# Performance work log

Hardware: AMD Instinct MI355X
Metric: run time of the kernel (lower is better)

## Reference

```python
import jax, jax.numpy as jnp
import numpy as np

B, S, D = 4, 2048, 1024
DFF = 512
E = 16
TOP_K = 2
N_SHARED = 2
FUSED_DFF = DFF * N_SHARED


def setup_inputs() -> dict:
    key = jax.random.key(0)
    ks = jax.random.split(key, 16)
    sc_d = 1.0 / np.sqrt(D)
    sc_f = 1.0 / np.sqrt(DFF)
    sc_sf = 1.0 / np.sqrt(FUSED_DFF)
    inp = {
        "x": jax.random.normal(ks[0], (B, S, D), dtype=jnp.float32),
        "gate_w": jax.random.uniform(ks[1], (E, D), dtype=jnp.float32, minval=-sc_d, maxval=sc_d),
        "expert_bias": jnp.zeros((E,), dtype=jnp.float32),
        # routed experts (SwiGLU): w1,w3: [E, DFF, D], w2: [E, D, DFF]
        "w1": jax.random.uniform(ks[2], (E, DFF, D), dtype=jnp.float32, minval=-sc_d, maxval=sc_d),
        "b1": jax.random.uniform(ks[3], (E, DFF), dtype=jnp.float32, minval=-sc_d, maxval=sc_d),
        "w3": jax.random.uniform(ks[4], (E, DFF, D), dtype=jnp.float32, minval=-sc_d, maxval=sc_d),
        "b3": jax.random.uniform(ks[5], (E, DFF), dtype=jnp.float32, minval=-sc_d, maxval=sc_d),
        "w2": jax.random.uniform(ks[6], (E, D, DFF), dtype=jnp.float32, minval=-sc_f, maxval=sc_f),
        "b2": jax.random.uniform(ks[7], (E, D), dtype=jnp.float32, minval=-sc_f, maxval=sc_f),
        # fused shared experts: d_model -> 2*d_ff -> d_model
        "sw1": jax.random.uniform(ks[8], (FUSED_DFF, D), dtype=jnp.float32, minval=-sc_d, maxval=sc_d),
        "sb1": jax.random.uniform(ks[9], (FUSED_DFF,), dtype=jnp.float32, minval=-sc_d, maxval=sc_d),
        "sw3": jax.random.uniform(ks[10], (FUSED_DFF, D), dtype=jnp.float32, minval=-sc_d, maxval=sc_d),
        "sb3": jax.random.uniform(ks[11], (FUSED_DFF,), dtype=jnp.float32, minval=-sc_d, maxval=sc_d),
        "sw2": jax.random.uniform(ks[12], (D, FUSED_DFF), dtype=jnp.float32, minval=-sc_sf, maxval=sc_sf),
        "sb2": jax.random.uniform(ks[13], (D,), dtype=jnp.float32, minval=-sc_sf, maxval=sc_sf),
    }
    return inp


def reference(x, gate_w, expert_bias, w1, b1, w2, b2, w3, b3,
              sw1, sb1, sw2, sb2, sw3, sb3):
    Bv, Sv, Dv = x.shape
    xf = x.reshape(-1, Dv)                                  # [T, D]
    # --- Gate (sigmoid scores, top-k over bias-adjusted logits) ---
    logits = xf @ gate_w.T                                  # [T, E]
    scores = jax.nn.sigmoid(logits)
    biased = logits + expert_bias.astype(logits.dtype)[None, :]
    _, topk_idx = jax.lax.top_k(biased, TOP_K)              # [T, K]
    topk_w = jnp.take_along_axis(scores, topk_idx, axis=-1) # [T, K]
    topk_w = topk_w / (topk_w.sum(-1, keepdims=True) + 1e-10)
    # dense per-token per-expert combine weight (zero for unselected) [T, E]
    gatew = (jax.nn.one_hot(topk_idx, E, dtype=xf.dtype) * topk_w[..., None]).sum(1)
    # --- Routed experts: equivalent to sort/dispatch/grouped-GEMM/combine ---
    y = jnp.zeros_like(xf)
    for e in range(E):
        h = jax.nn.silu(xf @ w1[e].T + b1[e]) * (xf @ w3[e].T + b3[e])  # [T, DFF]
        y = y + gatew[:, e:e + 1] * (h @ w2[e].T + b2[e])
    # --- Fused shared experts ---
    hs = jax.nn.silu(xf @ sw1.T + sb1) * (xf @ sw3.T + sb3)             # [T, 2*DFF]
    y = y + hs @ sw2.T + sb2
    return y.reshape(Bv, Sv, Dv)
```

## Files before the change

### kernel.cpp

```cpp
#include <hip/hip_runtime.h>
#include <cstdint>
#include <cstddef>

#define DEV static __device__ __forceinline__

constexpr int TT   = 8192;
constexpr int DD   = 1024;
constexpr int DFF  = 512;
constexpr int NE   = 16;
constexpr int FDFF = 1024;
constexpr int NSLOT = TT * 2;
constexpr int NSLOT_PAD = NSLOT + NE * 128;
constexpr int MAXT = NSLOT / 128 + NE;
constexpr int HB   = 64;

constexpr size_t XB_OFF   = 0;
constexpr size_t HS_OFF   = XB_OFF  + (size_t)TT * DD * 2;
constexpr size_t HR_OFF   = HS_OFF  + (size_t)TT * FDFF * 2;
constexpr size_t W1B_OFF  = HR_OFF  + (size_t)NSLOT_PAD * DFF * 2;
constexpr size_t W3B_OFF  = W1B_OFF + (size_t)NE * DFF * DD * 2;
constexpr size_t W2B_OFF  = W3B_OFF + (size_t)NE * DFF * DD * 2;
constexpr size_t SW1B_OFF = W2B_OFF + (size_t)NE * DD * DFF * 2;
constexpr size_t SW3B_OFF = SW1B_OFF + (size_t)FDFF * DD * 2;
constexpr size_t SW2B_OFF = SW3B_OFF + (size_t)FDFF * DD * 2;
constexpr size_t TKI_OFF  = SW2B_OFF + (size_t)DD * FDFF * 2;
constexpr size_t TKW_OFF  = TKI_OFF + (size_t)NSLOT * 4;
constexpr size_t STOK_OFF = TKW_OFF + (size_t)NSLOT * 4;
constexpr size_t SWT_OFF  = STOK_OFF + (size_t)NSLOT_PAD * 4;
constexpr size_t LRK_OFF  = SWT_OFF + (size_t)NSLOT_PAD * 4;
constexpr size_t BCN_OFF  = LRK_OFF + (size_t)NSLOT * 4;
constexpr size_t BB_OFF   = BCN_OFF + (size_t)HB * NE * 4;
constexpr size_t OFS_OFF  = BB_OFF + (size_t)HB * NE * 4;
constexpr size_t TEX_OFF  = OFS_OFF + 128;
constexpr size_t TM0_OFF  = TEX_OFF + (size_t)MAXT * 4;

typedef __bf16 bf16x8 __attribute__((ext_vector_type(8)));
typedef float  floatx4 __attribute__((ext_vector_type(4)));
typedef unsigned short u16t;

DEV unsigned f2bf2(float lo, float hi) {
    unsigned a = __builtin_bit_cast(unsigned, lo);
    unsigned b = __builtin_bit_cast(unsigned, hi);
    a += 0x7FFFu + ((a >> 16) & 1u);
    b += 0x7FFFu + ((b >> 16) & 1u);
    return (a >> 16) | (b & 0xFFFF0000u);
}
DEV u16t f2bf1(float f) {
    unsigned u = __builtin_bit_cast(unsigned, f);
    u += 0x7FFFu + ((u >> 16) & 1u);
    return (u16t)(u >> 16);
}
DEV uint4 pack8(float4 a, float4 b) {
    uint4 r;
    r.x = f2bf2(a.x, a.y); r.y = f2bf2(a.z, a.w);
    r.z = f2bf2(b.x, b.y); r.w = f2bf2(b.z, b.w);
    return r;
}
DEV floatx4 mfma16(bf16x8 a, bf16x8 b, floatx4 c) {
    return __builtin_amdgcn_mfma_f32_16x16x32_bf16(a, b, c, 0, 0, 0);
}
DEV void glds16(const u16t* g, u16t* l) {
    __builtin_amdgcn_global_load_lds(
        (const __attribute__((address_space(1))) unsigned int*)g,
        (__attribute__((address_space(3))) unsigned int*)l, 16, 0, 0);
}
DEV float dot4(float4 a, float4 b) { return a.x*b.x + a.y*b.y + a.z*b.z + a.w*b.w; }

__global__ __launch_bounds__(256) void k_cvtw(
        const float* __restrict__ w1, const float* __restrict__ w3, const float* __restrict__ w2,
        const float* __restrict__ sw1, const float* __restrict__ sw3, const float* __restrict__ sw2,
        u16t* __restrict__ w1b, u16t* __restrict__ w3b, u16t* __restrict__ w2b,
        u16t* __restrict__ sw1b, u16t* __restrict__ sw3b, u16t* __restrict__ sw2b) {
    int b = blockIdx.x;
    const float* src; u16t* dst; size_t base;
    if      (b < 4096)  { src = w1;  dst = w1b;  base = (size_t)b * 2048; }
    else if (b < 8192)  { src = w3;  dst = w3b;  base = (size_t)(b - 4096) * 2048; }
    else if (b < 12288) { src = w2;  dst = w2b;  base = (size_t)(b - 8192) * 2048; }
    else if (b < 12800) { src = sw1; dst = sw1b; base = (size_t)(b - 12288) * 2048; }
    else if (b < 13312) { src = sw3; dst = sw3b; base = (size_t)(b - 12800) * 2048; }
    else                { src = sw2; dst = sw2b; base = (size_t)(b - 13312) * 2048; }
    size_t i = base + (size_t)threadIdx.x * 8;
    float4 a = *(const float4*)(src + i);
    float4 c = *(const float4*)(src + i + 4);
    *(uint4*)(dst + i) = pack8(a, c);
}

__global__ __launch_bounds__(256) void k_cvtx(const float* __restrict__ x, u16t* __restrict__ xb) {
    size_t i = ((size_t)blockIdx.x * 256 + threadIdx.x) * 8;
    float4 a = *(const float4*)(x + i);
    float4 b = *(const float4*)(x + i + 4);
    *(uint4*)(xb + i) = pack8(a, b);
}

__global__ __launch_bounds__(256) void k_gate(const float* __restrict__ x,
                                              const float* __restrict__ gw,
                                              const float* __restrict__ eb,
                                              int* __restrict__ tki, float* __restrict__ tkw) {
    const int tid = threadIdx.x;
    const int wave = tid >> 6, lane = tid & 63;
    const int tok0 = blockIdx.x * 16 + wave * 4;
    float acc[4][16];
#pragma unroll
    for (int t = 0; t < 4; t++)
#pragma unroll
        for (int e = 0; e < 16; e++) acc[t][e] = 0.f;
#pragma unroll
    for (int i = 0; i < 4; i++) {
        const int d = i * 256 + lane * 4;
        float4 xv[4];
#pragma unroll
        for (int t = 0; t < 4; t++) xv[t] = *(const float4*)(x + (size_t)(tok0 + t) * DD + d);
#pragma unroll
        for (int e = 0; e < 16; e++) {
            float4 wv = *(const float4*)(gw + (size_t)e * DD + d);
#pragma unroll
            for (int t = 0; t < 4; t++) acc[t][e] += dot4(xv[t], wv);
        }
    }
#pragma unroll
    for (int t = 0; t < 4; t++)
#pragma unroll
        for (int e = 0; e < 16; e++) {
            float v = acc[t][e];
            v += __shfl_xor(v, 1);  v += __shfl_xor(v, 2);  v += __shfl_xor(v, 4);
            v += __shfl_xor(v, 8);  v += __shfl_xor(v, 16); v += __shfl_xor(v, 32);
            acc[t][e] = v;
        }
    if (lane == 0) {
        float ebs[16];
#pragma unroll
        for (int e = 0; e < 16; e++) ebs[e] = eb[e];
#pragma unroll
        for (int t = 0; t < 4; t++) {
            float b0 = -1e30f, b1v = -1e30f, l0 = 0.f, l1 = 0.f;
            int i0 = 0, i1 = 0;
#pragma unroll
            for (int e = 0; e < 16; e++) {
                float lv = acc[t][e];
                float bl = lv + ebs[e];
                if (bl > b0)       { b1v = b0; i1 = i0; l1 = l0; b0 = bl; i0 = e; l0 = lv; }
                else if (bl > b1v) { b1v = bl; i1 = e; l1 = lv; }
            }
            float s0 = 1.f / (1.f + expf(-l0));
            float s1 = 1.f / (1.f + expf(-l1));
            float dn = s0 + s1 + 1e-10f;
            int tok = tok0 + t;
            tki[tok * 2] = i0; tki[tok * 2 + 1] = i1;
            tkw[tok * 2] = s0 / dn; tkw[tok * 2 + 1] = s1 / dn;
        }
    }
}

__global__ __launch_bounds__(256) void k_hist(const int* __restrict__ tki,
                                              int* __restrict__ lrank, int* __restrict__ bcnt) {
    __shared__ int h[NE];
    const int tid = threadIdx.x;
    if (tid < NE) h[tid] = 0;
    __syncthreads();
    int idx = blockIdx.x * 256 + tid;
    int e = tki[idx];
    lrank[idx] = atomicAdd(&h[e], 1);
    __syncthreads();
    if (tid < NE) bcnt[blockIdx.x * NE + tid] = h[tid];
}

__global__ void k_scan(const int* __restrict__ bcnt, int* __restrict__ offs,
                       int* __restrict__ bb, int* __restrict__ texp, int* __restrict__ tm0) {
    __shared__ int cntS[NE], offS[NE];
    const int tid = threadIdx.x;
    if (tid < NE) {
        int s = 0;
#pragma unroll
        for (int b = 0; b < HB; b++) s += bcnt[b * NE + tid];
        cntS[tid] = s;
    }
    __syncthreads();
    if (tid == 0) {
        int off = 0, t = 0;
        for (int e = 0; e < NE; e++) {
            offS[e] = off; offs[e] = off;
            int nt = (cntS[e] + 127) >> 7;
            for (int i = 0; i < nt; i++) { texp[t] = e; tm0[t] = off + i * 128; t++; }
            off += nt * 128;
        }
        offs[NE] = off;
        for (; t < MAXT; t++) texp[t] = -1;
    }
    __syncthreads();
    if (tid < NE) {
        int run = offS[tid];
        for (int b = 0; b < HB; b++) { bb[b * NE + tid] = run; run += bcnt[b * NE + tid]; }
    }
}

__global__ __launch_bounds__(256) void k_scatter(const int* __restrict__ tki,
                                                 const float* __restrict__ tkw,
                                                 const int* __restrict__ bb,
                                                 const int* __restrict__ lrank,
                                                 int* __restrict__ stok, float* __restrict__ swt) {
    int idx = blockIdx.x * 256 + threadIdx.x;
    int e = tki[idx];
    int slot = bb[blockIdx.x * NE + e] + lrank[idx];
    stok[slot] = idx >> 1;
    swt[slot] = tkw[idx];
}

__global__ __launch_bounds__(256) void k_sgemm1(const u16t* __restrict__ xb,
        const u16t* __restrict__ w1b, const float* __restrict__ sb1,
        const u16t* __restrict__ w3b, const float* __restrict__ sb3,
        u16t* __restrict__ Hs) {
    __shared__ u16t As[128 * 32], B1s[64 * 32], B3s[64 * 32];
    const int m0 = blockIdx.x * 128, n0 = blockIdx.y * 64;
    const int tid = threadIdx.x, lane = tid & 63, wid = tid >> 6;
    const int wm = (wid & 1) * 64, wn = (wid >> 1) * 32;
    const int q = lane >> 4, r = lane & 15;
    const int srow = tid >> 2, scg = (tid & 3) * 8;
    floatx4 acc1[4][2], acc3[4][2];
#pragma unroll
    for (int i = 0; i < 4; i++)
#pragma unroll
        for (int j = 0; j < 2; j++) { acc1[i][j] = (floatx4)0.f; acc3[i][j] = (floatx4)0.f; }
    const u16t* a0  = xb  + (size_t)(m0 + srow) * DD + scg;
    const u16t* a1  = xb  + (size_t)(m0 + 64 + srow) * DD + scg;
    const u16t* b1g = w1b + (size_t)(n0 + srow) * DD + scg;
    const u16t* b3g = w3b + (size_t)(n0 + srow) * DD + scg;
    u16t* lA0 = As + tid * 8;
    u16t* lA1 = As + 2048 + tid * 8;
    u16t* lB1 = B1s + tid * 8;
    u16t* lB3 = B3s + tid * 8;
    for (int k0 = 0; k0 < DD; k0 += 32) {
        glds16(a0 + k0, lA0); glds16(a1 + k0, lA1);
        glds16(b1g + k0, lB1); glds16(b3g + k0, lB3);
        __syncthreads();
        bf16x8 af[4], f1[2], f3[2];
#pragma unroll
        for (int i = 0; i < 4; i++) af[i] = *(const bf16x8*)&As[(wm + i * 16 + r) * 32 + q * 8];
#pragma unroll
        for (int j = 0; j < 2; j++) {
            f1[j] = *(const bf16x8*)&B1s[(wn + j * 16 + r) * 32 + q * 8];
            f3[j] = *(const bf16x8*)&B3s[(wn + j * 16 + r) * 32 + q * 8];
        }
#pragma unroll
        for (int i = 0; i < 4; i++)
#pragma unroll
            for (int j = 0; j < 2; j++) {
                acc1[i][j] = mfma16(af[i], f1[j], acc1[i][j]);
                acc3[i][j] = mfma16(af[i], f3[j], acc3[i][j]);
            }
        __syncthreads();
    }
    float s1v[2], s3v[2];
#pragma unroll
    for (int j = 0; j < 2; j++) {
        int col = n0 + wn + j * 16 + r;
        s1v[j] = sb1[col]; s3v[j] = sb3[col];
    }
#pragma unroll
    for (int i = 0; i < 4; i++)
#pragma unroll
        for (int j = 0; j < 2; j++)
#pragma unroll
            for (int g = 0; g < 4; g++) {
                int row = m0 + wm + i * 16 + q * 4 + g;
                int col = n0 + wn + j * 16 + r;
                float z1 = acc1[i][j][g] + s1v[j];
                float z3 = acc3[i][j][g] + s3v[j];
                float h = (z1 / (1.f + __expf(-z1))) * z3;
                Hs[(size_t)row * FDFF + col] = f2bf1(h);
            }
}

__global__ __launch_bounds__(256) void k_sgemm2(const u16t* __restrict__ Hs,
        const u16t* __restrict__ sw2b, const float* __restrict__ sb2,
        float* __restrict__ out) {
    __shared__ u16t As[128 * 32], Bs[128 * 32];
    const int m0 = blockIdx.x * 128, n0 = blockIdx.y * 128;
    const int tid = threadIdx.x, lane = tid & 63, wid = tid >> 6;
    const int wm = (wid & 1) * 64, wn = (wid >> 1) * 64;
    const int q = lane >> 4, r = lane & 15;
    const int srow = tid >> 2, scg = (tid & 3) * 8;
    floatx4 acc[4][4];
#pragma unroll
    for (int i = 0; i < 4; i++)
#pragma unroll
        for (int j = 0; j < 4; j++) acc[i][j] = (floatx4)0.f;
    const u16t* a0 = Hs + (size_t)(m0 + srow) * FDFF + scg;
    const u16t* a1 = Hs + (size_t)(m0 + 64 + srow) * FDFF + scg;
    const u16t* b0 = sw2b + (size_t)(n0 + srow) * FDFF + scg;
    const u16t* b1 = sw2b + (size_t)(n0 + 64 + srow) * FDFF + scg;
    u16t* lA0 = As + tid * 8;       u16t* lA1 = As + 2048 + tid * 8;
    u16t* lB0 = Bs + tid * 8;       u16t* lB1 = Bs + 2048 + tid * 8;
    for (int k0 = 0; k0 < FDFF; k0 += 32) {
        glds16(a0 + k0, lA0); glds16(a1 + k0, lA1);
        glds16(b0 + k0, lB0); glds16(b1 + k0, lB1);
        __syncthreads();
        bf16x8 af[4], bf[4];
#pragma unroll
        for (int i = 0; i < 4; i++) af[i] = *(const bf16x8*)&As[(wm + i * 16 + r) * 32 + q * 8];
#pragma unroll
        for (int j = 0; j < 4; j++) bf[j] = *(const bf16x8*)&Bs[(wn + j * 16 + r) * 32 + q * 8];
#pragma unroll
        for (int i = 0; i < 4; i++)
#pragma unroll
            for (int j = 0; j < 4; j++) acc[i][j] = mfma16(af[i], bf[j], acc[i][j]);
        __syncthreads();
    }
    float bv[4];
#pragma unroll
    for (int j = 0; j < 4; j++) bv[j] = sb2[n0 + wn + j * 16 + r];
#pragma unroll
    for (int i = 0; i < 4; i++)
#pragma unroll
        for (int j = 0; j < 4; j++)
#pragma unroll
            for (int g = 0; g < 4; g++) {
                int row = m0 + wm + i * 16 + q * 4 + g;
                int col = n0 + wn + j * 16 + r;
                out[(size_t)row * DD + col] = acc[i][j][g] + bv[j];
            }
}

__global__ __launch_bounds__(256) void k_rgemm1(const u16t* __restrict__ xb,
        const u16t* __restrict__ w1b, const float* __restrict__ b1,
        const u16t* __restrict__ w3b, const float* __restrict__ b3,
        const int* __restrict__ stok,
        const int* __restrict__ texp, const int* __restrict__ tm0,
        u16t* __restrict__ Hr) {
    const int te = texp[blockIdx.x];
    if (te < 0) return;
    const int m0 = tm0[blockIdx.x], n0 = blockIdx.y * 64;
    __shared__ u16t As[128 * 32], B1s[64 * 32], B3s[64 * 32];
    __shared__ int toksS[128];
    const int tid = threadIdx.x, lane = tid & 63, wid = tid >> 6;
    const int wm = (wid & 1) * 64, wn = (wid >> 1) * 32;
    const int q = lane >> 4, r = lane & 15;
    const int srow = tid >> 2, scg = (tid & 3) * 8;
    if (tid < 128) { int t = stok[m0 + tid]; toksS[tid] = t < 0 ? 0 : t; }
    __syncthreads();
    floatx4 acc1[4][2], acc3[4][2];
#pragma unroll
    for (int i = 0; i < 4; i++)
#pragma unroll
        for (int j = 0; j < 2; j++) { acc1[i][j] = (floatx4)0.f; acc3[i][j] = (floatx4)0.f; }
    const u16t* a0  = xb + (size_t)toksS[srow] * DD + scg;
    const u16t* a1  = xb + (size_t)toksS[64 + srow] * DD + scg;
    const u16t* b1g = w1b + (size_t)te * DFF * DD + (size_t)(n0 + srow) * DD + scg;
    const u16t* b3g = w3b + (size_t)te * DFF * DD + (size_t)(n0 + srow) * DD + scg;
    const float* b1e = b1 + (size_t)te * DFF;
    const float* b3e = b3 + (size_t)te * DFF;
    u16t* lA0 = As + tid * 8;
    u16t* lA1 = As + 2048 + tid * 8;
    u16t* lB1 = B1s + tid * 8;
    u16t* lB3 = B3s + tid * 8;
    for (int k0 = 0; k0 < DD; k0 += 32) {
        glds16(a0 + k0, lA0); glds16(a1 + k0, lA1);
        glds16(b1g + k0, lB1); glds16(b3g + k0, lB3);
        __syncthreads();
        bf16x8 af[4], f1[2], f3[2];
#pragma unroll
        for (int i = 0; i < 4; i++) af[i] = *(const bf16x8*)&As[(wm + i * 16 + r) * 32 + q * 8];
#pragma unroll
        for (int j = 0; j < 2; j++) {
            f1[j] = *(const bf16x8*)&B1s[(wn + j * 16 + r) * 32 + q * 8];
            f3[j] = *(const bf16x8*)&B3s[(wn + j * 16 + r) * 32 + q * 8];
        }
#pragma unroll
        for (int i = 0; i < 4; i++)
#pragma unroll
            for (int j = 0; j < 2; j++) {
                acc1[i][j] = mfma16(af[i], f1[j], acc1[i][j]);
                acc3[i][j] = mfma16(af[i], f3[j], acc3[i][j]);
            }
        __syncthreads();
    }
    float s1v[2], s3v[2];
#pragma unroll
    for (int j = 0; j < 2; j++) {
        int col = n0 + wn + j * 16 + r;
        s1v[j] = b1e[col]; s3v[j] = b3e[col];
    }
#pragma unroll
    for (int i = 0; i < 4; i++)
#pragma unroll
        for (int j = 0; j < 2; j++)
#pragma unroll
            for (int g = 0; g < 4; g++) {
                int slot = m0 + wm + i * 16 + q * 4 + g;
                int col = n0 + wn + j * 16 + r;
                float z1 = acc1[i][j][g] + s1v[j];
                float z3 = acc3[i][j][g] + s3v[j];
                float h = (z1 / (1.f + __expf(-z1))) * z3;
                Hr[(size_t)slot * DFF + col] = f2bf1(h);
            }
}

__global__ __launch_bounds__(256) void k_rgemm2(const u16t* __restrict__ Hr,
        const u16t* __restrict__ w2b, const float* __restrict__ b2,
        const int* __restrict__ stok, const float* __restrict__ swt,
        const int* __restrict__ texp, const int* __restrict__ tm0,
        float* __restrict__ out) {
    const int te = texp[blockIdx.x];
    if (te < 0) return;
    const int m0 = tm0[blockIdx.x], n0 = blockIdx.y * 128;
    __shared__ u16t As[128 * 32], Bs[128 * 32];
    __shared__ int toksR[128];
    __shared__ float swtL[128];
    const int tid = threadIdx.x, lane = tid & 63, wid = tid >> 6;
    const int wm = (wid & 1) * 64, wn = (wid >> 1) * 64;
    const int q = lane >> 4, r = lane & 15;
    const int srow = tid >> 2, scg = (tid & 3) * 8;
    if (tid < 128) { toksR[tid] = stok[m0 + tid]; swtL[tid] = swt[m0 + tid]; }
    floatx4 acc[4][4];
#pragma unroll
    for (int i = 0; i < 4; i++)
#pragma unroll
        for (int j = 0; j < 4; j++) acc[i][j] = (floatx4)0.f;
    const u16t* a0 = Hr + (size_t)(m0 + srow) * DFF + scg;
    const u16t* a1 = Hr + (size_t)(m0 + 64 + srow) * DFF + scg;
    const u16t* b0 = w2b + (size_t)te * DD * DFF + (size_t)(n0 + srow) * DFF + scg;
    const u16t* b1 = w2b + (size_t)te * DD * DFF + (size_t)(n0 + 64 + srow) * DFF + scg;
    const float* b2e = b2 + (size_t)te * DD;
    u16t* lA0 = As + tid * 8;       u16t* lA1 = As + 2048 + tid * 8;
    u16t* lB0 = Bs + tid * 8;       u16t* lB1 = Bs + 2048 + tid * 8;
    for (int k0 = 0; k0 < DFF; k0 += 32) {
        glds16(a0 + k0, lA0); glds16(a1 + k0, lA1);
        glds16(b0 + k0, lB0); glds16(b1 + k0, lB1);
        __syncthreads();
        bf16x8 af[4], bf[4];
#pragma unroll
        for (int i = 0; i < 4; i++) af[i] = *(const bf16x8*)&As[(wm + i * 16 + r) * 32 + q * 8];
#pragma unroll
        for (int j = 0; j < 4; j++) bf[j] = *(const bf16x8*)&Bs[(wn + j * 16 + r) * 32 + q * 8];
#pragma unroll
        for (int i = 0; i < 4; i++)
#pragma unroll
            for (int j = 0; j < 4; j++) acc[i][j] = mfma16(af[i], bf[j], acc[i][j]);
        __syncthreads();
    }
    float bv[4];
#pragma unroll
    for (int j = 0; j < 4; j++) bv[j] = b2e[n0 + wn + j * 16 + r];
#pragma unroll
    for (int i = 0; i < 4; i++)
#pragma unroll
        for (int g = 0; g < 4; g++) {
            int rowl = wm + i * 16 + q * 4 + g;
            int tk = toksR[rowl];
            if (tk >= 0) {
                float gwv = swtL[rowl];
#pragma unroll
                for (int j = 0; j < 4; j++) {
                    int col = n0 + wn + j * 16 + r;
                    atomicAdd(out + (size_t)tk * DD + col, gwv * (acc[i][j][g] + bv[j]));
                }
            }
        }
}

extern "C" void kernel_launch(void* const* d_in, const int* in_sizes, int n_in,
                              void* d_out, int out_size, void* d_ws, size_t ws_size,
                              hipStream_t stream) {
    const float* x   = (const float*)d_in[0];
    const float* gw  = (const float*)d_in[1];
    const float* eb  = (const float*)d_in[2];
    const float* w1  = (const float*)d_in[3];
    const float* b1  = (const float*)d_in[4];
    const float* w3  = (const float*)d_in[5];
    const float* b3  = (const float*)d_in[6];
    const float* w2  = (const float*)d_in[7];
    const float* b2  = (const float*)d_in[8];
    const float* sw1 = (const float*)d_in[9];
    const float* sb1 = (const float*)d_in[10];
    const float* sw3 = (const float*)d_in[11];
    const float* sb3 = (const float*)d_in[12];
    const float* sw2 = (const float*)d_in[13];
    const float* sb2 = (const float*)d_in[14];
    float* out = (float*)d_out;
    char* ws = (char*)d_ws;

    u16t*  xb   = (u16t*)(ws + XB_OFF);
    u16t*  Hs   = (u16t*)(ws + HS_OFF);
    u16t*  Hr   = (u16t*)(ws + HR_OFF);
    u16t*  w1b  = (u16t*)(ws + W1B_OFF);
    u16t*  w3b  = (u16t*)(ws + W3B_OFF);
    u16t*  w2b  = (u16t*)(ws + W2B_OFF);
    u16t*  sw1b = (u16t*)(ws + SW1B_OFF);
    u16t*  sw3b = (u16t*)(ws + SW3B_OFF);
    u16t*  sw2b = (u16t*)(ws + SW2B_OFF);
    int*   tki  = (int*)(ws + TKI_OFF);
    float* tkw  = (float*)(ws + TKW_OFF);
    int*   stok = (int*)(ws + STOK_OFF);
    float* swt  = (float*)(ws + SWT_OFF);
    int*   lrank = (int*)(ws + LRK_OFF);
    int*   bcnt = (int*)(ws + BCN_OFF);
    int*   bb   = (int*)(ws + BB_OFF);
    int*   offs = (int*)(ws + OFS_OFF);
    int*   texp = (int*)(ws + TEX_OFF);
    int*   tm0  = (int*)(ws + TM0_OFF);

    hipMemsetAsync(stok, 0xFF, (size_t)NSLOT_PAD * 4, stream);

    k_cvtw<<<13824, 256, 0, stream>>>(w1, w3, w2, sw1, sw3, sw2, w1b, w3b, w2b, sw1b, sw3b, sw2b);
    k_cvtx<<<4096, 256, 0, stream>>>(x, xb);
    k_gate<<<512, 256, 0, stream>>>(x, gw, eb, tki, tkw);
    k_hist<<<HB, 256, 0, stream>>>(tki, lrank, bcnt);
    k_scan<<<1, 64, 0, stream>>>(bcnt, offs, bb, texp, tm0);
    k_scatter<<<HB, 256, 0, stream>>>(tki, tkw, bb, lrank, stok, swt);

    k_sgemm1<<<dim3(TT / 128, FDFF / 64), 256, 0, stream>>>(xb, sw1b, sb1, sw3b, sb3, Hs);
    k_sgemm2<<<dim3(TT / 128, DD / 128), 256, 0, stream>>>(Hs, sw2b, sb2, out);
    k_rgemm1<<<dim3(MAXT, DFF / 64), 256, 0, stream>>>(xb, w1b, b1, w3b, b3, stok, texp, tm0, Hr);
    k_rgemm2<<<dim3(MAXT, DD / 128), 256, 0, stream>>>(Hr, w2b, b2, stok, swt, texp, tm0, out);
}
```

Measured before the change: 462.0 us.

## Swizzle LDS tile layout for conflict-free fragment reads; replace atomic combine with gather kernel

The global-to-LDS load mapping is changed so each 16-row group is stored contiguously by k-chunk, letting the MFMA fragment reads hit consecutive addresses instead of 64-byte-strided rows. This targets LDS bank conflicts in all four GEMM kernels. In addition, the routed down-projection now writes bf16 per-slot results to a new buffer. A separate combine kernel then gathers each token's two slots, applies bias and gate weights, and adds them to the output without float atomics. The trade is an extra intermediate buffer write/read, one more launch, and bf16 rounding of the routed output before combining.

```diff
diff --git a/kernel.cpp b/kernel.cpp
--- a/kernel.cpp
+++ b/kernel.cpp
@@ -17,7 +17,8 @@
 constexpr size_t XB_OFF   = 0;
 constexpr size_t HS_OFF   = XB_OFF  + (size_t)TT * DD * 2;
 constexpr size_t HR_OFF   = HS_OFF  + (size_t)TT * FDFF * 2;
-constexpr size_t W1B_OFF  = HR_OFF  + (size_t)NSLOT_PAD * DFF * 2;
+constexpr size_t YR_OFF   = HR_OFF  + (size_t)NSLOT_PAD * DFF * 2;
+constexpr size_t W1B_OFF  = YR_OFF  + (size_t)NSLOT_PAD * DD * 2;
 constexpr size_t W3B_OFF  = W1B_OFF + (size_t)NE * DFF * DD * 2;
 constexpr size_t W2B_OFF  = W3B_OFF + (size_t)NE * DFF * DD * 2;
 constexpr size_t SW1B_OFF = W2B_OFF + (size_t)NE * DD * DFF * 2;
@@ -26,8 +27,8 @@
 constexpr size_t TKI_OFF  = SW2B_OFF + (size_t)DD * FDFF * 2;
 constexpr size_t TKW_OFF  = TKI_OFF + (size_t)NSLOT * 4;
 constexpr size_t STOK_OFF = TKW_OFF + (size_t)NSLOT * 4;
-constexpr size_t SWT_OFF  = STOK_OFF + (size_t)NSLOT_PAD * 4;
-constexpr size_t LRK_OFF  = SWT_OFF + (size_t)NSLOT_PAD * 4;
+constexpr size_t PSL_OFF  = STOK_OFF + (size_t)NSLOT_PAD * 4;
+constexpr size_t LRK_OFF  = PSL_OFF + (size_t)NSLOT * 4;
 constexpr size_t BCN_OFF  = LRK_OFF + (size_t)NSLOT * 4;
 constexpr size_t BB_OFF   = BCN_OFF + (size_t)HB * NE * 4;
 constexpr size_t OFS_OFF  = BB_OFF + (size_t)HB * NE * 4;
@@ -50,6 +51,7 @@
     u += 0x7FFFu + ((u >> 16) & 1u);
     return (u16t)(u >> 16);
 }
+DEV float bf2f(u16t v) { unsigned u = (unsigned)v << 16; return __builtin_bit_cast(float, u); }
 DEV uint4 pack8(float4 a, float4 b) {
     uint4 r;
     r.x = f2bf2(a.x, a.y); r.y = f2bf2(a.z, a.w);
@@ -194,16 +196,18 @@
 }
 
 __global__ __launch_bounds__(256) void k_scatter(const int* __restrict__ tki,
-                                                 const float* __restrict__ tkw,
                                                  const int* __restrict__ bb,
                                                  const int* __restrict__ lrank,
-                                                 int* __restrict__ stok, float* __restrict__ swt) {
+                                                 int* __restrict__ stok, int* __restrict__ pslot) {
     int idx = blockIdx.x * 256 + threadIdx.x;
     int e = tki[idx];
     int slot = bb[blockIdx.x * NE + e] + lrank[idx];
     stok[slot] = idx >> 1;
-    swt[slot] = tkw[idx];
-}
+    pslot[idx] = slot;
+}
+
+#define LROW(tid) ((((tid) >> 6) << 4) | ((tid) & 15))
+#define LCG(tid)  ((((tid) >> 4) & 3) * 8)
 
 __global__ __launch_bounds__(256) void k_sgemm1(const u16t* __restrict__ xb,
         const u16t* __restrict__ w1b, const float* __restrict__ sb1,
@@ -214,31 +218,32 @@
     const int tid = threadIdx.x, lane = tid & 63, wid = tid >> 6;
     const int wm = (wid & 1) * 64, wn = (wid >> 1) * 32;
     const int q = lane >> 4, r = lane & 15;
-    const int srow = tid >> 2, scg = (tid & 3) * 8;
+    const int lrow = LROW(tid), lcg = LCG(tid);
     floatx4 acc1[4][2], acc3[4][2];
 #pragma unroll
     for (int i = 0; i < 4; i++)
 #pragma unroll
         for (int j = 0; j < 2; j++) { acc1[i][j] = (floatx4)0.f; acc3[i][j] = (floatx4)0.f; }
-    const u16t* a0  = xb  + (size_t)(m0 + srow) * DD + scg;
-    const u16t* a1  = xb  + (size_t)(m0 + 64 + srow) * DD + scg;
-    const u16t* b1g = w1b + (size_t)(n0 + srow) * DD + scg;
-    const u16t* b3g = w3b + (size_t)(n0 + srow) * DD + scg;
+    const u16t* a0  = xb  + (size_t)(m0 + lrow) * DD + lcg;
+    const u16t* a1  = xb  + (size_t)(m0 + 64 + lrow) * DD + lcg;
+    const u16t* b1g = w1b + (size_t)(n0 + lrow) * DD + lcg;
+    const u16t* b3g = w3b + (size_t)(n0 + lrow) * DD + lcg;
     u16t* lA0 = As + tid * 8;
     u16t* lA1 = As + 2048 + tid * 8;
     u16t* lB1 = B1s + tid * 8;
     u16t* lB3 = B3s + tid * 8;
+    const int ag = (wm >> 4), bg = (wn >> 4);
     for (int k0 = 0; k0 < DD; k0 += 32) {
         glds16(a0 + k0, lA0); glds16(a1 + k0, lA1);
         glds16(b1g + k0, lB1); glds16(b3g + k0, lB3);
         __syncthreads();
         bf16x8 af[4], f1[2], f3[2];
 #pragma unroll
-        for (int i = 0; i < 4; i++) af[i] = *(const bf16x8*)&As[(wm + i * 16 + r) * 32 + q * 8];
+        for (int i = 0; i < 4; i++) af[i] = *(const bf16x8*)&As[(ag + i) * 512 + q * 128 + r * 8];
 #pragma unroll
         for (int j = 0; j < 2; j++) {
-            f1[j] = *(const bf16x8*)&B1s[(wn + j * 16 + r) * 32 + q * 8];
-            f3[j] = *(const bf16x8*)&B3s[(wn + j * 16 + r) * 32 + q * 8];
+            f1[j] = *(const bf16x8*)&B1s[(bg + j) * 512 + q * 128 + r * 8];
+            f3[j] = *(const bf16x8*)&B3s[(bg + j) * 512 + q * 128 + r * 8];
         }
 #pragma unroll
         for (int i = 0; i < 4; i++)
@@ -278,27 +283,28 @@
     const int tid = threadIdx.x, lane = tid & 63, wid = tid >> 6;
     const int wm = (wid & 1) * 64, wn = (wid >> 1) * 64;
     const int q = lane >> 4, r = lane & 15;
-    const int srow = tid >> 2, scg = (tid & 3) * 8;
+    const int lrow = LROW(tid), lcg = LCG(tid);
     floatx4 acc[4][4];
 #pragma unroll
     for (int i = 0; i < 4; i++)
 #pragma unroll
         for (int j = 0; j < 4; j++) acc[i][j] = (floatx4)0.f;
-    const u16t* a0 = Hs + (size_t)(m0 + srow) * FDFF + scg;
-    const u16t* a1 = Hs + (size_t)(m0 + 64 + srow) * FDFF + scg;
-    const u16t* b0 = sw2b + (size_t)(n0 + srow) * FDFF + scg;
-    const u16t* b1 = sw2b + (size_t)(n0 + 64 + srow) * FDFF + scg;
+    const u16t* a0 = Hs + (size_t)(m0 + lrow) * FDFF + lcg;
+    const u16t* a1 = Hs + (size_t)(m0 + 64 + lrow) * FDFF + lcg;
+    const u16t* b0 = sw2b + (size_t)(n0 + lrow) * FDFF + lcg;
+    const u16t* b1 = sw2b + (size_t)(n0 + 64 + lrow) * FDFF + lcg;
     u16t* lA0 = As + tid * 8;       u16t* lA1 = As + 2048 + tid * 8;
     u16t* lB0 = Bs + tid * 8;       u16t* lB1 = Bs + 2048 + tid * 8;
+    const int ag = (wm >> 4), bg = (wn >> 4);
     for (int k0 = 0; k0 < FDFF; k0 += 32) {
         glds16(a0 + k0, lA0); glds16(a1 + k0, lA1);
         glds16(b0 + k0, lB0); glds16(b1 + k0, lB1);
         __syncthreads();
         bf16x8 af[4], bf[4];
 #pragma unroll
-        for (int i = 0; i < 4; i++) af[i] = *(const bf16x8*)&As[(wm + i * 16 + r) * 32 + q * 8];
-#pragma unroll
-        for (int j = 0; j < 4; j++) bf[j] = *(const bf16x8*)&Bs[(wn + j * 16 + r) * 32 + q * 8];
+        for (int i = 0; i < 4; i++) af[i] = *(const bf16x8*)&As[(ag + i) * 512 + q * 128 + r * 8];
+#pragma unroll
+        for (int j = 0; j < 4; j++) bf[j] = *(const bf16x8*)&Bs[(bg + j) * 512 + q * 128 + r * 8];
 #pragma unroll
         for (int i = 0; i < 4; i++)
 #pragma unroll
@@ -334,7 +340,7 @@
     const int tid = threadIdx.x, lane = tid & 63, wid = tid >> 6;
     const int wm = (wid & 1) * 64, wn = (wid >> 1) * 32;
     const int q = lane >> 4, r = lane & 15;
-    const int srow = tid >> 2, scg = (tid & 3) * 8;
+    const int lrow = LROW(tid), lcg = LCG(tid);
     if (tid < 128) { int t = stok[m0 + tid]; toksS[tid] = t < 0 ? 0 : t; }
     __syncthreads();
     floatx4 acc1[4][2], acc3[4][2];
@@ -342,27 +348,28 @@
     for (int i = 0; i < 4; i++)
 #pragma unroll
         for (int j = 0; j < 2; j++) { acc1[i][j] = (floatx4)0.f; acc3[i][j] = (floatx4)0.f; }
-    const u16t* a0  = xb + (size_t)toksS[srow] * DD + scg;
-    const u16t* a1  = xb + (size_t)toksS[64 + srow] * DD + scg;
-    const u16t* b1g = w1b + (size_t)te * DFF * DD + (size_t)(n0 + srow) * DD + scg;
-    const u16t* b3g = w3b + (size_t)te * DFF * DD + (size_t)(n0 + srow) * DD + scg;
+    const u16t* a0  = xb + (size_t)toksS[lrow] * DD + lcg;
+    const u16t* a1  = xb + (size_t)toksS[64 + lrow] * DD + lcg;
+    const u16t* b1g = w1b + (size_t)te * DFF * DD + (size_t)(n0 + lrow) * DD + lcg;
+    const u16t* b3g = w3b + (size_t)te * DFF * DD + (size_t)(n0 + lrow) * DD + lcg;
     const float* b1e = b1 + (size_t)te * DFF;
     const float* b3e = b3 + (size_t)te * DFF;
     u16t* lA0 = As + tid * 8;
     u16t* lA1 = As + 2048 + tid * 8;
     u16t* lB1 = B1s + tid * 8;
     u16t* lB3 = B3s + tid * 8;
+    const int ag = (wm >> 4), bg = (wn >> 4);
     for (int k0 = 0; k0 < DD; k0 += 32) {
         glds16(a0 + k0, lA0); glds16(a1 + k0, lA1);
         glds16(b1g + k0, lB1); glds16(b3g + k0, lB3);
         __syncthreads();
         bf16x8 af[4], f1[2], f3[2];
 #pragma unroll
-        for (int i = 0; i < 4; i++) af[i] = *(const bf16x8*)&As[(wm + i * 16 + r) * 32 + q * 8];
+        for (int i = 0; i < 4; i++) af[i] = *(const bf16x8*)&As[(ag + i) * 512 + q * 128 + r * 8];
 #pragma unroll
         for (int j = 0; j < 2; j++) {
-            f1[j] = *(const bf16x8*)&B1s[(wn + j * 16 + r) * 32 + q * 8];
-            f3[j] = *(const bf16x8*)&B3s[(wn + j * 16 + r) * 32 + q * 8];
+            f1[j] = *(const bf16x8*)&B1s[(bg + j) * 512 + q * 128 + r * 8];
+            f3[j] = *(const bf16x8*)&B3s[(bg + j) * 512 + q * 128 + r * 8];
         }
 #pragma unroll
         for (int i = 0; i < 4; i++)
@@ -395,66 +402,75 @@
 }
 
 __global__ __launch_bounds__(256) void k_rgemm2(const u16t* __restrict__ Hr,
-        const u16t* __restrict__ w2b, const float* __restrict__ b2,
-        const int* __restrict__ stok, const float* __restrict__ swt,
+        const u16t* __restrict__ w2b,
         const int* __restrict__ texp, const int* __restrict__ tm0,
-        float* __restrict__ out) {
+        u16t* __restrict__ Yr) {
     const int te = texp[blockIdx.x];
     if (te < 0) return;
     const int m0 = tm0[blockIdx.x], n0 = blockIdx.y * 128;
     __shared__ u16t As[128 * 32], Bs[128 * 32];
-    __shared__ int toksR[128];
-    __shared__ float swtL[128];
     const int tid = threadIdx.x, lane = tid & 63, wid = tid >> 6;
     const int wm = (wid & 1) * 64, wn = (wid >> 1) * 64;
     const int q = lane >> 4, r = lane & 15;
-    const int srow = tid >> 2, scg = (tid & 3) * 8;
-    if (tid < 128) { toksR[tid] = stok[m0 + tid]; swtL[tid] = swt[m0 + tid]; }
+    const int lrow = LROW(tid), lcg = LCG(tid);
     floatx4 acc[4][4];
 #pragma unroll
     for (int i = 0; i < 4; i++)
 #pragma unroll
         for (int j = 0; j < 4; j++) acc[i][j] = (floatx4)0.f;
-    const u16t* a0 = Hr + (size_t)(m0 + srow) * DFF + scg;
-    const u16t* a1 = Hr + (size_t)(m0 + 64 + srow) * DFF + scg;
-    const u16t* b0 = w2b + (size_t)te * DD * DFF + (size_t)(n0 + srow) * DFF + scg;
-    const u16t* b1 = w2b + (size_t)te * DD * DFF + (size_t)(n0 + 64 + srow) * DFF + scg;
-    const float* b2e = b2 + (size_t)te * DD;
+    const u16t* a0 = Hr + (size_t)(m0 + lrow) * DFF + lcg;
+    const u16t* a1 = Hr + (size_t)(m0 + 64 + lrow) * DFF + lcg;
+    const u16t* b0 = w2b + (size_t)te * DD * DFF + (size_t)(n0 + lrow) * DFF + lcg;
+    const u16t* b1 = w2b + (size_t)te * DD * DFF + (size_t)(n0 + 64 + lrow) * DFF + lcg;
     u16t* lA0 = As + tid * 8;       u16t* lA1 = As + 2048 + tid * 8;
     u16t* lB0 = Bs + tid * 8;       u16t* lB1 = Bs + 2048 + tid * 8;
+    const int ag = (wm >> 4), bg = (wn >> 4);
     for (int k0 = 0; k0 < DFF; k0 += 32) {
         glds16(a0 + k0, lA0); glds16(a1 + k0, lA1);
         glds16(b0 + k0, lB0); glds16(b1 + k0, lB1);
         __syncthreads();
         bf16x8 af[4], bf[4];
 #pragma unroll
-        for (int i = 0; i < 4; i++) af[i] = *(const bf16x8*)&As[(wm + i * 16 + r) * 32 + q * 8];
-#pragma unroll
-        for (int j = 0; j < 4; j++) bf[j] = *(const bf16x8*)&Bs[(wn + j * 16 + r) * 32 + q * 8];
+        for (int i = 0; i < 4; i++) af[i] = *(const bf16x8*)&As[(ag + i) * 512 + q * 128 + r * 8];
+#pragma unroll
+        for (int j = 0; j < 4; j++) bf[j] = *(const bf16x8*)&Bs[(bg + j) * 512 + q * 128 + r * 8];
 #pragma unroll
         for (int i = 0; i < 4; i++)
 #pragma unroll
             for (int j = 0; j < 4; j++) acc[i][j] = mfma16(af[i], bf[j], acc[i][j]);
         __syncthreads();
     }
-    float bv[4];
-#pragma unroll
-    for (int j = 0; j < 4; j++) bv[j] = b2e[n0 + wn + j * 16 + r];
-#pragma unroll
-    for (int i = 0; i < 4; i++)
-#pragma unroll
-        for (int g = 0; g < 4; g++) {
-            int rowl = wm + i * 16 + q * 4 + g;
-            int tk = toksR[rowl];
-            if (tk >= 0) {
-                float gwv = swtL[rowl];
-#pragma unroll
-                for (int j = 0; j < 4; j++) {
-                    int col = n0 + wn + j * 16 + r;
-                    atomicAdd(out + (size_t)tk * DD + col, gwv * (acc[i][j][g] + bv[j]));
-                }
-            }
-        }
+#pragma unroll
+    for (int i = 0; i < 4; i++)
+#pragma unroll
+        for (int j = 0; j < 4; j++)
+#pragma unroll
+            for (int g = 0; g < 4; g++) {
+                int slot = m0 + wm + i * 16 + q * 4 + g;
+                int col = n0 + wn + j * 16 + r;
+                Yr[(size_t)slot * DD + col] = f2bf1(acc[i][j][g]);
+            }
+}
+
+__global__ __launch_bounds__(256) void k_comb(const u16t* __restrict__ Yr,
+        const float* __restrict__ b2,
+        const int* __restrict__ pslot, const int* __restrict__ tki,
+        const float* __restrict__ tkw, float* __restrict__ out) {
+    const int t = blockIdx.x;
+    const int c = threadIdx.x * 4;
+    const int s0 = pslot[2 * t], s1 = pslot[2 * t + 1];
+    const int e0 = tki[2 * t], e1 = tki[2 * t + 1];
+    const float w0 = tkw[2 * t], w1 = tkw[2 * t + 1];
+    float4 o = *(float4*)(out + (size_t)t * DD + c);
+    ushort4 y0 = *(const ushort4*)(Yr + (size_t)s0 * DD + c);
+    ushort4 y1 = *(const ushort4*)(Yr + (size_t)s1 * DD + c);
+    float4 p0 = *(const float4*)(b2 + (size_t)e0 * DD + c);
+    float4 p1 = *(const float4*)(b2 + (size_t)e1 * DD + c);
+    o.x += w0 * (bf2f(y0.x) + p0.x) + w1 * (bf2f(y1.x) + p1.x);
+    o.y += w0 * (bf2f(y0.y) + p0.y) + w1 * (bf2f(y1.y) + p1.y);
+    o.z += w0 * (bf2f(y0.z) + p0.z) + w1 * (bf2f(y1.z) + p1.z);
+    o.w += w0 * (bf2f(y0.w) + p0.w) + w1 * (bf2f(y1.w) + p1.w);
+    *(float4*)(out + (size_t)t * DD + c) = o;
 }
 
 extern "C" void kernel_launch(void* const* d_in, const int* in_sizes, int n_in,
@@ -481,6 +497,7 @@
     u16t*  xb   = (u16t*)(ws + XB_OFF);
     u16t*  Hs   = (u16t*)(ws + HS_OFF);
     u16t*  Hr   = (u16t*)(ws + HR_OFF);
+    u16t*  Yr   = (u16t*)(ws + YR_OFF);
     u16t*  w1b  = (u16t*)(ws + W1B_OFF);
     u16t*  w3b  = (u16t*)(ws + W3B_OFF);
     u16t*  w2b  = (u16t*)(ws + W2B_OFF);
@@ -490,7 +507,7 @@
     int*   tki  = (int*)(ws + TKI_OFF);
     float* tkw  = (float*)(ws + TKW_OFF);
     int*   stok = (int*)(ws + STOK_OFF);
-    float* swt  = (float*)(ws + SWT_OFF);
+    int*   pslot = (int*)(ws + PSL_OFF);
     int*   lrank = (int*)(ws + LRK_OFF);
     int*   bcnt = (int*)(ws + BCN_OFF);
     int*   bb   = (int*)(ws + BB_OFF);
@@ -505,10 +522,11 @@
     k_gate<<<512, 256, 0, stream>>>(x, gw, eb, tki, tkw);
     k_hist<<<HB, 256, 0, stream>>>(tki, lrank, bcnt);
     k_scan<<<1, 64, 0, stream>>>(bcnt, offs, bb, texp, tm0);
-    k_scatter<<<HB, 256, 0, stream>>>(tki, tkw, bb, lrank, stok, swt);
+    k_scatter<<<HB, 256, 0, stream>>>(tki, bb, lrank, stok, pslot);
 
     k_sgemm1<<<dim3(TT / 128, FDFF / 64), 256, 0, stream>>>(xb, sw1b, sb1, sw3b, sb3, Hs);
     k_sgemm2<<<dim3(TT / 128, DD / 128), 256, 0, stream>>>(Hs, sw2b, sb2, out);
     k_rgemm1<<<dim3(MAXT, DFF / 64), 256, 0, stream>>>(xb, w1b, b1, w3b, b3, stok, texp, tm0, Hr);
-    k_rgemm2<<<dim3(MAXT, DD / 128), 256, 0, stream>>>(Hr, w2b, b2, stok, swt, texp, tm0, out);
-}
+    k_rgemm2<<<dim3(MAXT, DD / 128), 256, 0, stream>>>(Hr, w2b, texp, tm0, Yr);
+    k_comb<<<TT, 256, 0, stream>>>(Yr, b2, pslot, tki, tkw, out);
+}
```

New measurement: 513.8 us. 1.11x slower.
